# Performance work log

Measured on AMD Instinct MI355X. Metric: run time of the kernel, lower is better.

The kernel has to match this reference:

```python
import jax, jax.numpy as jnp
import numpy as np

B, S, D, K, R = 64, 512, 768, 8, 277
D_K = 64  # attention scale dim from original module (self.d_k)


def setup_inputs() -> dict:
    key = jax.random.key(0)
    ks = jax.random.split(key, 10)
    sc = 1.0 / np.sqrt(D)
    return {
        "embedding": jax.random.normal(ks[0], (B, S, D), dtype=jnp.float32),
        "h_span": jnp.sort(jax.random.randint(ks[1], (B, 2), 0, S), axis=-1).astype(jnp.int32),
        "t_span": jnp.sort(jax.random.randint(ks[2], (B, 2), 0, S), axis=-1).astype(jnp.int32),
        "b_spans": jnp.sort(jax.random.randint(ks[3], (B, K, 2), 0, S), axis=-1).astype(jnp.int32),
        "wu_w": jax.random.normal(ks[4], (D, D), dtype=jnp.float32) * sc,
        "wu_b": jnp.zeros((D,), jnp.float32),
        "wv_w": jax.random.normal(ks[5], (D, D), dtype=jnp.float32) * sc,
        "wv_b": jnp.zeros((D,), jnp.float32),
        "wi_w": jax.random.normal(ks[6], (D, D), dtype=jnp.float32) * sc,
        "wi_b": jnp.zeros((D,), jnp.float32),
        "ln1_w": jax.random.normal(ks[7], (D, D), dtype=jnp.float32) * sc,
        "ln1_b": jnp.zeros((D,), jnp.float32),
        "pred_w": jax.random.normal(ks[8], (R, D), dtype=jnp.float32) * sc,
        "pred_b": jnp.zeros((R,), jnp.float32),
    }


def _span_max(emb, span):
    # emb: [B, S, D]; span: [B, 2] inclusive [start, end] (start <= end).
    pos = jnp.arange(emb.shape[1])[None, :]          # [1, S]
    m = (pos >= span[:, :1]) & (pos <= span[:, 1:])  # [B, S]
    return jnp.max(jnp.where(m[:, :, None], emb, -jnp.inf), axis=1)  # [B, D]


def reference(embedding, h_span, t_span, b_spans,
              wu_w, wu_b, wv_w, wv_b, wi_w, wi_b,
              ln1_w, ln1_b, pred_w, pred_b):
    # Ragged entity-span max-pooling (torch.max over embedding[dp, s:e+1]).
    h_emb = _span_max(embedding, h_span)   # [B, D]
    t_emb = _span_max(embedding, t_span)   # [B, D]
    # K is a small fixed structural count (bridge subsampling cap); loop is fine.
    b_emb = jnp.stack([_span_max(embedding, b_spans[:, k, :]) for k in range(K)], axis=1)  # [B, K, D]

    # wu/wv/wi attention-style multi-hop path aggregation.
    u = h_emb @ wu_w.T + wu_b              # [B, D]
    v = t_emb @ wv_w.T + wv_b              # [B, D]
    bi = jnp.einsum('bkd,ed->bke', b_emb, wi_w) + wi_b  # [B, K, D]
    att = jax.nn.softmax(jnp.einsum('bd,bkd->bk', u, bi) / np.sqrt(D_K), axis=-1)  # [B, K]
    ctx = jnp.einsum('bk,bkd->bd', att, bi)  # [B, D]

    pair = jax.nn.relu((u + v + ctx) @ ln1_w.T + ln1_b)  # [B, D]
    logits = pair @ pred_w.T + pred_b                    # [B, R]
    return logits
```

## Files before the change

kernel.cpp:

```cpp
#include <hip/hip_runtime.h>
#include <hip/hip_bf16.h>

#define B 64
#define S 512
#define D 768
#define K 8
#define R 277
#define NSPAN 10
#define M_TOT 640

typedef unsigned short ushort_t;
typedef __attribute__((ext_vector_type(8))) short short8;
typedef __attribute__((ext_vector_type(4))) float f32x4;

__device__ __forceinline__ ushort_t f2bf(float f) {
    unsigned u = __float_as_uint(f);
    unsigned r = (u + 0x7FFFu + ((u >> 16) & 1u)) >> 16;
    return (ushort_t)r;
}

template<int RPC, int NCH>
__global__ void k_pool1(const float* __restrict__ emb,
                        const int* __restrict__ h_span,
                        const int* __restrict__ t_span,
                        const int* __restrict__ b_spans,
                        const float* __restrict__ wu,
                        const float* __restrict__ wv,
                        const float* __restrict__ wi,
                        float* __restrict__ partial,
                        ushort_t* __restrict__ wbf) {
    int b = blockIdx.x, c = blockIdx.y;
    int t = threadIdx.x;

    if (c >= NCH) {
        int g = (b * 18 + (c - NCH)) * 192 + t;
        const int per = (D*D) / 8;
        if (g < 3*per) {
            const float* src = (g < per) ? wu : (g < 2*per) ? wv : wi;
            int lg = g - ((g < per) ? 0 : (g < 2*per) ? per : 2*per);
            float4 f0 = *(const float4*)(src + (size_t)lg*8);
            float4 f1 = *(const float4*)(src + (size_t)lg*8 + 4);
            short8 o;
            o[0] = (short)f2bf(f0.x); o[1] = (short)f2bf(f0.y);
            o[2] = (short)f2bf(f0.z); o[3] = (short)f2bf(f0.w);
            o[4] = (short)f2bf(f1.x); o[5] = (short)f2bf(f1.y);
            o[6] = (short)f2bf(f1.z); o[7] = (short)f2bf(f1.w);
            *(short8*)&wbf[(size_t)g * 8] = o;
        }
        return;
    }

    int r0 = c * RPC;
    int s0[NSPAN], s1[NSPAN];
    s0[0] = h_span[b*2]; s1[0] = h_span[b*2+1];
    s0[1] = t_span[b*2]; s1[1] = t_span[b*2+1];
    #pragma unroll
    for (int k = 0; k < K; ++k) {
        s0[2+k] = b_spans[(b*K+k)*2];
        s1[2+k] = b_spans[(b*K+k)*2 + 1];
    }

    bool any = false;
    #pragma unroll
    for (int j = 0; j < NSPAN; ++j)
        any |= (s1[j] >= r0) && (s0[j] < r0 + RPC);
    if (!any) return;

    float4 m[NSPAN];
    #pragma unroll
    for (int j = 0; j < NSPAN; ++j)
        m[j] = make_float4(-INFINITY, -INFINITY, -INFINITY, -INFINITY);

    const float4* e4 = (const float4*)(emb + (size_t)b * S * D) + (size_t)r0 * (D/4) + t;
    #pragma unroll
    for (int i = 0; i < RPC; ++i) {
        float4 v = e4[i * (D/4)];
        int s = r0 + i;
        #pragma unroll
        for (int j = 0; j < NSPAN; ++j) {
            bool in = (s >= s0[j]) && (s <= s1[j]);
            float vx = in ? v.x : -INFINITY;
            float vy = in ? v.y : -INFINITY;
            float vz = in ? v.z : -INFINITY;
            float vw = in ? v.w : -INFINITY;
            m[j].x = fmaxf(m[j].x, vx); m[j].y = fmaxf(m[j].y, vy);
            m[j].z = fmaxf(m[j].z, vz); m[j].w = fmaxf(m[j].w, vw);
        }
    }

    #pragma unroll
    for (int j = 0; j < NSPAN; ++j) {
        if (s1[j] >= r0 && s0[j] < r0 + RPC) {
            *(float4*)(partial + (((size_t)(b*NCH + c))*NSPAN + j) * D + t*4) = m[j];
        }
    }
}

__global__ void k_pool2(const float* __restrict__ partial,
                        const int* __restrict__ h_span,
                        const int* __restrict__ t_span,
                        const int* __restrict__ b_spans,
                        ushort_t* __restrict__ pooled_bf, int rpc) {
    int task = blockIdx.x;
    int b = task / NSPAN, j = task % NSPAN;
    int s0, s1, row;
    if (j == 0)      { s0 = h_span[b*2]; s1 = h_span[b*2+1]; row = b; }
    else if (j == 1) { s0 = t_span[b*2]; s1 = t_span[b*2+1]; row = B + b; }
    else {
        int k = j - 2;
        s0 = b_spans[(b*K+k)*2]; s1 = b_spans[(b*K+k)*2 + 1];
        row = 2*B + b*K + k;
    }
    int nch = S / rpc;
    int c0 = s0 / rpc, c1 = s1 / rpc;
    int t = threadIdx.x;
    float4 m = make_float4(-INFINITY, -INFINITY, -INFINITY, -INFINITY);
    for (int c = c0; c <= c1; ++c) {
        float4 v = *(const float4*)(partial + (((size_t)(b*nch + c))*NSPAN + j) * D + t*4);
        m.x = fmaxf(m.x, v.x); m.y = fmaxf(m.y, v.y);
        m.z = fmaxf(m.z, v.z); m.w = fmaxf(m.w, v.w);
    }
    unsigned lo = (unsigned)f2bf(m.x) | ((unsigned)f2bf(m.y) << 16);
    unsigned hi = (unsigned)f2bf(m.z) | ((unsigned)f2bf(m.w) << 16);
    *(uint2*)&pooled_bf[(size_t)row * D + t*4] = make_uint2(lo, hi);
}

template<int KSPLIT>
__global__ __launch_bounds__(256)
void k_gemm_bf(const ushort_t* __restrict__ abf,
               const ushort_t* __restrict__ wbf,
               float* __restrict__ p_part) {
    __shared__ ushort_t Al[64][64];
    __shared__ ushort_t Bl[64][64];
    int e0 = blockIdx.x * 64;
    int m0 = blockIdx.y * 64;
    int dbase = blockIdx.z * (D / KSPLIT);
    const ushort_t* Wm = wbf + (size_t)((m0 < B) ? 0 : (m0 < 2*B) ? 1 : 2) * D * D;

    int tid = threadIdx.x;
    int w = tid >> 6, l = tid & 63;
    int srow = tid >> 2;
    int sc   = tid & 3;

    const ushort_t* ga = abf + (size_t)(m0 + srow) * D + dbase;
    const ushort_t* gb = Wm  + (size_t)(e0 + srow) * D + dbase;
    int p0 = ((sc     ) ^ (srow & 7)) * 8;
    int p1 = ((sc + 4 ) ^ (srow & 7)) * 8;

    f32x4 acc[4] = {};
    const int NIT = (D / KSPLIT) / 64;
    short8 pa0 = *(const short8*)(ga + sc*8);
    short8 pa1 = *(const short8*)(ga + sc*8 + 32);
    short8 pb0 = *(const short8*)(gb + sc*8);
    short8 pb1 = *(const short8*)(gb + sc*8 + 32);

    for (int it = 0; it < NIT; ++it) {
        __syncthreads();
        *(short8*)&Al[srow][p0] = pa0;
        *(short8*)&Al[srow][p1] = pa1;
        *(short8*)&Bl[srow][p0] = pb0;
        *(short8*)&Bl[srow][p1] = pb1;
        __syncthreads();
        if (it + 1 < NIT) {
            ga += 64; gb += 64;
            pa0 = *(const short8*)(ga + sc*8);
            pa1 = *(const short8*)(ga + sc*8 + 32);
            pb0 = *(const short8*)(gb + sc*8);
            pb1 = *(const short8*)(gb + sc*8 + 32);
        }
        int g = l >> 4, x = l & 7;
        #pragma unroll
        for (int ks = 0; ks < 2; ++ks) {
            int chunk = ks*4 + g;
            short8 a = *(const short8*)&Al[w*16 + (l & 15)][(chunk ^ x) * 8];
            #pragma unroll
            for (int nt = 0; nt < 4; ++nt) {
                short8 bf = *(const short8*)&Bl[nt*16 + (l & 15)][(chunk ^ x) * 8];
                acc[nt] = __builtin_amdgcn_mfma_f32_16x16x32_bf16(a, bf, acc[nt], 0, 0, 0);
            }
        }
    }

    int r4 = (l >> 4) * 4, cc = l & 15;
    #pragma unroll
    for (int nt = 0; nt < 4; ++nt)
        #pragma unroll
        for (int r = 0; r < 4; ++r)
            p_part[((size_t)blockIdx.z * M_TOT + m0 + w*16 + r4 + r) * D + e0 + nt*16 + cc] = acc[nt][r];
}

template<int KSPLIT>
__global__ __launch_bounds__(512)
void k_att2(const float* __restrict__ p_part,
            const float* __restrict__ wu_b,
            const float* __restrict__ wv_b,
            const float* __restrict__ wi_b,
            const float* __restrict__ pred_b,
            float* __restrict__ s_out,
            float* __restrict__ out) {
    __shared__ float U[D], V[D], BI[K][D];
    __shared__ float dots[K];
    int b = blockIdx.x, tid = threadIdx.x;

    for (int r = tid; r < R; r += 512) out[(size_t)b * R + r] = pred_b[r];

    for (int task = tid; task < NSPAN * (D/4); task += 512) {
        int j = task / (D/4), sl = task % (D/4);
        size_t row = (j == 0) ? (size_t)b : (j == 1) ? (size_t)(B + b)
                   : (size_t)(2*B + b*K + (j - 2));
        const float* bias = (j == 0) ? wu_b : (j == 1) ? wv_b : wi_b;
        float4 acc = *(const float4*)(bias + sl*4);
        #pragma unroll
        for (int ks = 0; ks < KSPLIT; ++ks) {
            float4 p = *(const float4*)(p_part + ((size_t)ks * M_TOT + row) * D + sl*4);
            acc.x += p.x; acc.y += p.y; acc.z += p.z; acc.w += p.w;
        }
        float* dst = (j == 0) ? U : (j == 1) ? V : BI[j-2];
        *(float4*)(dst + sl*4) = acc;
    }
    __syncthreads();

    int wave = tid >> 6, lane = tid & 63;
    {
        float part = 0.f;
        #pragma unroll
        for (int i = 0; i < D/64; ++i) {
            int d = i*64 + lane;
            part += U[d] * BI[wave][d];
        }
        #pragma unroll
        for (int off = 32; off > 0; off >>= 1) part += __shfl_xor(part, off);
        if (lane == 0) dots[wave] = part * 0.125f;
    }
    __syncthreads();

    float mx = -INFINITY;
    #pragma unroll
    for (int k = 0; k < K; ++k) mx = fmaxf(mx, dots[k]);
    float ex[K], sum = 0.f;
    #pragma unroll
    for (int k = 0; k < K; ++k) { ex[k] = expf(dots[k] - mx); sum += ex[k]; }
    float inv = 1.f / sum;
    for (int d = tid; d < D; d += 512) {
        float c = 0.f;
        #pragma unroll
        for (int k = 0; k < K; ++k) c += ex[k] * BI[k][d];
        s_out[(size_t)b * D + d] = U[d] + V[d] + c * inv;
    }
}

__device__ __forceinline__
void tile_fma(const float (*At)[68], const float (*Wt)[68],
              int tx, int ty, float acc[4][4]) {
    #pragma unroll
    for (int dd = 0; dd < 16; ++dd) {
        float4 av  = *(const float4*)&At[dd][ty << 2];
        float4 wvv = *(const float4*)&Wt[dd][tx << 2];
        float a_[4] = {av.x, av.y, av.z, av.w};
        float w_[4] = {wvv.x, wvv.y, wvv.z, wvv.w};
        #pragma unroll
        for (int i = 0; i < 4; ++i)
            #pragma unroll
            for (int jj = 0; jj < 4; ++jj)
                acc[i][jj] += a_[i] * w_[jj];
    }
}

template<int KS>
__global__ void k_pairg(const float* __restrict__ s,
                        const float* __restrict__ ln1_w,
                        float* __restrict__ pair_part) {
    __shared__ float At[16][68];
    __shared__ float Wt[16][68];
    int e0 = blockIdx.x * 64;
    int dbase = blockIdx.y * (D / KS);

    int tid = threadIdx.x;
    int tx = tid & 15, ty = tid >> 4;
    int lm = tid >> 2;
    int ld = (tid & 3) * 4;

    const float* arow = s     + (size_t)lm * D + ld + dbase;
    const float* wrow = ln1_w + (size_t)(e0 + lm) * D + ld + dbase;

    float acc[4][4] = {};
    const int NK = (D/KS) / 16;
    float4 a4 = *(const float4*)(arow);
    float4 w4 = *(const float4*)(wrow);
    for (int kc = 0; kc < NK; ++kc) {
        __syncthreads();
        At[ld+0][lm] = a4.x; At[ld+1][lm] = a4.y; At[ld+2][lm] = a4.z; At[ld+3][lm] = a4.w;
        Wt[ld+0][lm] = w4.x; Wt[ld+1][lm] = w4.y; Wt[ld+2][lm] = w4.z; Wt[ld+3][lm] = w4.w;
        __syncthreads();
        if (kc + 1 < NK) {
            a4 = *(const float4*)(arow + (kc+1)*16);
            w4 = *(const float4*)(wrow + (kc+1)*16);
        }
        tile_fma(At, Wt, tx, ty, acc);
    }
    #pragma unroll
    for (int i = 0; i < 4; ++i) {
        float4 o = make_float4(acc[i][0], acc[i][1], acc[i][2], acc[i][3]);
        *(float4*)(pair_part + ((size_t)blockIdx.y * B + ty*4 + i) * D + e0 + tx*4) = o;
    }
}

template<int KSP, int KSPAIR>
__global__ void k_predg(const float* __restrict__ pair_part,
                        const float* __restrict__ ln1_b,
                        const float* __restrict__ pred_w,
                        float* __restrict__ out) {
    __shared__ float At[16][68];
    __shared__ float Wt[16][68];
    int r0 = blockIdx.x * 64;
    int dbase = blockIdx.y * (D / KSP);

    int tid = threadIdx.x;
    int tx = tid & 15, ty = tid >> 4;
    int lm = tid >> 2;
    int ld = (tid & 3) * 4;

    int rw = r0 + lm; if (rw >= R) rw = R - 1;
    const float* prow = pair_part + (size_t)lm * D + ld + dbase;
    const float* wrow = pred_w + (size_t)rw * D + ld + dbase;

    auto build_a = [&](int kc) -> float4 {
        float4 a = *(const float4*)(ln1_b + dbase + kc*16 + ld);
        #pragma unroll
        for (int ks = 0; ks < KSPAIR; ++ks) {
            float4 p = *(const float4*)(prow + (size_t)ks * B * D + kc*16);
            a.x += p.x; a.y += p.y; a.z += p.z; a.w += p.w;
        }
        a.x = fmaxf(a.x, 0.f); a.y = fmaxf(a.y, 0.f);
        a.z = fmaxf(a.z, 0.f); a.w = fmaxf(a.w, 0.f);
        return a;
    };

    float acc[4][4] = {};
    const int NK = (D/KSP) / 16;
    float4 a4 = build_a(0);
    float4 w4 = *(const float4*)(wrow);
    for (int kc = 0; kc < NK; ++kc) {
        __syncthreads();
        At[ld+0][lm] = a4.x; At[ld+1][lm] = a4.y; At[ld+2][lm] = a4.z; At[ld+3][lm] = a4.w;
        Wt[ld+0][lm] = w4.x; Wt[ld+1][lm] = w4.y; Wt[ld+2][lm] = w4.z; Wt[ld+3][lm] = w4.w;
        __syncthreads();
        if (kc + 1 < NK) {
            a4 = build_a(kc+1);
            w4 = *(const float4*)(wrow + (kc+1)*16);
        }
        tile_fma(At, Wt, tx, ty, acc);
    }
    #pragma unroll
    for (int i = 0; i < 4; ++i) {
        int m = ty*4 + i;
        #pragma unroll
        for (int jj = 0; jj < 4; ++jj) {
            int r = r0 + tx*4 + jj;
            if (r < R) atomicAdd(&out[(size_t)m * R + r], acc[i][jj]);
        }
    }
}

extern "C" void kernel_launch(void* const* d_in, const int* in_sizes, int n_in,
                              void* d_out, int out_size, void* d_ws, size_t ws_size,
                              hipStream_t stream) {
    const float* emb     = (const float*)d_in[0];
    const int*   h_span  = (const int*)  d_in[1];
    const int*   t_span  = (const int*)  d_in[2];
    const int*   b_spans = (const int*)  d_in[3];
    const float* wu_w    = (const float*)d_in[4];
    const float* wu_b    = (const float*)d_in[5];
    const float* wv_w    = (const float*)d_in[6];
    const float* wv_b    = (const float*)d_in[7];
    const float* wi_w    = (const float*)d_in[8];
    const float* wi_b    = (const float*)d_in[9];
    const float* ln1_w   = (const float*)d_in[10];
    const float* ln1_b   = (const float*)d_in[11];
    const float* pred_w  = (const float*)d_in[12];
    const float* pred_b  = (const float*)d_in[13];
    float* out = (float*)d_out;

    const int KSPLIT = 2;
    const int KS     = 8;
    const int NCH    = 32;

    float* ws = (float*)d_ws;
    ushort_t* pooled_bf = (ushort_t*)ws;
    ushort_t* wbf   = (ushort_t*)(ws + (size_t)M_TOT*D/2);
    float* p_part    = ws + (size_t)M_TOT*D/2 + (size_t)3*D*D/2;
    float* s_buf     = p_part + (size_t)KSPLIT * M_TOT * D;
    float* pair_part = s_buf + (size_t)B * D;
    float* partial   = pair_part + (size_t)KS * B * D;
    (void)ws_size; (void)in_sizes; (void)n_in; (void)out_size;

    k_pool1<S/NCH, NCH><<<dim3(B, NCH + 18), 192, 0, stream>>>(
        emb, h_span, t_span, b_spans, wu_w, wv_w, wi_w, partial, wbf);
    k_pool2<<<M_TOT, 192, 0, stream>>>(partial, h_span, t_span, b_spans, pooled_bf, S / NCH);
    k_gemm_bf<KSPLIT><<<dim3(D/64, M_TOT/64, KSPLIT), 256, 0, stream>>>(pooled_bf, wbf, p_part);
    k_att2<KSPLIT><<<B, 512, 0, stream>>>(p_part, wu_b, wv_b, wi_b, pred_b, s_buf, out);
    k_pairg<KS><<<dim3(D/64, KS), 256, 0, stream>>>(s_buf, ln1_w, pair_part);
    k_predg<KS, KS><<<dim3((R+63)/64, KS), 256, 0, stream>>>(pair_part, ln1_b, pred_w, out);
}
```

Before: 66.07 us.

## Convert pair and prediction GEMMs to bf16 MFMA with fused weight conversion

Replaces the fp32 scalar-FMA tiled GEMMs for the ln1 and pred layers with bf16 MFMA kernels. The ln1_w and pred_w weights are converted to bf16 in the existing conversion blocks of the pooling kernel, and the attention output is now written as bf16. The split-K factors change to 6 and 12. The aim is to cut ALU time on the two tail GEMMs, at the cost of extra per-call conversion traffic and reduced precision.

After: 55.57 us. -15.9%, faster.

```diff
diff --git a/kernel.cpp b/kernel.cpp
--- a/kernel.cpp
+++ b/kernel.cpp
@@ -8,6 +8,7 @@
 #define R 277
 #define NSPAN 10
 #define M_TOT 640
+#define DD (D*D)
 
 typedef unsigned short ushort_t;
 typedef __attribute__((ext_vector_type(8))) short short8;
@@ -19,7 +20,7 @@
     return (ushort_t)r;
 }
 
-template<int RPC, int NCH>
+template<int RPC, int NCH, int CVTY>
 __global__ void k_pool1(const float* __restrict__ emb,
                         const int* __restrict__ h_span,
                         const int* __restrict__ t_span,
@@ -27,25 +28,32 @@
                         const float* __restrict__ wu,
                         const float* __restrict__ wv,
                         const float* __restrict__ wi,
+                        const float* __restrict__ ln1_w,
+                        const float* __restrict__ pred_w,
                         float* __restrict__ partial,
                         ushort_t* __restrict__ wbf) {
     int b = blockIdx.x, c = blockIdx.y;
     int t = threadIdx.x;
 
     if (c >= NCH) {
-        int g = (b * 18 + (c - NCH)) * 192 + t;
-        const int per = (D*D) / 8;
-        if (g < 3*per) {
-            const float* src = (g < per) ? wu : (g < 2*per) ? wv : wi;
-            int lg = g - ((g < per) ? 0 : (g < 2*per) ? per : 2*per);
-            float4 f0 = *(const float4*)(src + (size_t)lg*8);
-            float4 f1 = *(const float4*)(src + (size_t)lg*8 + 4);
+        int g = (b * CVTY + (c - NCH)) * 192 + t;
+        size_t e0 = (size_t)g * 8;
+        const size_t TOT = (size_t)4*DD + (size_t)R*D;
+        if (e0 < TOT) {
+            const float* src; size_t off;
+            if      (e0 < (size_t)DD)   { src = wu;     off = e0; }
+            else if (e0 < (size_t)2*DD) { src = wv;     off = e0 - DD; }
+            else if (e0 < (size_t)3*DD) { src = wi;     off = e0 - (size_t)2*DD; }
+            else if (e0 < (size_t)4*DD) { src = ln1_w;  off = e0 - (size_t)3*DD; }
+            else                        { src = pred_w; off = e0 - (size_t)4*DD; }
+            float4 f0 = *(const float4*)(src + off);
+            float4 f1 = *(const float4*)(src + off + 4);
             short8 o;
             o[0] = (short)f2bf(f0.x); o[1] = (short)f2bf(f0.y);
             o[2] = (short)f2bf(f0.z); o[3] = (short)f2bf(f0.w);
             o[4] = (short)f2bf(f1.x); o[5] = (short)f2bf(f1.y);
             o[6] = (short)f2bf(f1.z); o[7] = (short)f2bf(f1.w);
-            *(short8*)&wbf[(size_t)g * 8] = o;
+            *(short8*)&wbf[e0] = o;
         }
         return;
     }
@@ -135,7 +143,7 @@
     int e0 = blockIdx.x * 64;
     int m0 = blockIdx.y * 64;
     int dbase = blockIdx.z * (D / KSPLIT);
-    const ushort_t* Wm = wbf + (size_t)((m0 < B) ? 0 : (m0 < 2*B) ? 1 : 2) * D * D;
+    const ushort_t* Wm = wbf + (size_t)((m0 < B) ? 0 : (m0 < 2*B) ? 1 : 2) * DD;
 
     int tid = threadIdx.x;
     int w = tid >> 6, l = tid & 63;
@@ -196,7 +204,7 @@
             const float* __restrict__ wv_b,
             const float* __restrict__ wi_b,
             const float* __restrict__ pred_b,
-            float* __restrict__ s_out,
+            ushort_t* __restrict__ s_bf,
             float* __restrict__ out) {
     __shared__ float U[D], V[D], BI[K][D];
     __shared__ float dots[K];
@@ -245,119 +253,143 @@
         float c = 0.f;
         #pragma unroll
         for (int k = 0; k < K; ++k) c += ex[k] * BI[k][d];
-        s_out[(size_t)b * D + d] = U[d] + V[d] + c * inv;
-    }
-}
-
-__device__ __forceinline__
-void tile_fma(const float (*At)[68], const float (*Wt)[68],
-              int tx, int ty, float acc[4][4]) {
-    #pragma unroll
-    for (int dd = 0; dd < 16; ++dd) {
-        float4 av  = *(const float4*)&At[dd][ty << 2];
-        float4 wvv = *(const float4*)&Wt[dd][tx << 2];
-        float a_[4] = {av.x, av.y, av.z, av.w};
-        float w_[4] = {wvv.x, wvv.y, wvv.z, wvv.w};
-        #pragma unroll
-        for (int i = 0; i < 4; ++i)
+        s_bf[(size_t)b * D + d] = f2bf(U[d] + V[d] + c * inv);
+    }
+}
+
+template<int KSPL>
+__global__ __launch_bounds__(256)
+void k_pairg_bf(const ushort_t* __restrict__ s_bf,
+                const ushort_t* __restrict__ ln1_bf,
+                float* __restrict__ pair_part) {
+    __shared__ ushort_t Al[64][64];
+    __shared__ ushort_t Bl[64][64];
+    int e0 = blockIdx.x * 64;
+    int dbase = blockIdx.y * (D / KSPL);
+
+    int tid = threadIdx.x;
+    int w = tid >> 6, l = tid & 63;
+    int srow = tid >> 2;
+    int sc   = tid & 3;
+
+    const ushort_t* ga = s_bf   + (size_t)srow * D + dbase;
+    const ushort_t* gb = ln1_bf + (size_t)(e0 + srow) * D + dbase;
+    int p0 = ((sc     ) ^ (srow & 7)) * 8;
+    int p1 = ((sc + 4 ) ^ (srow & 7)) * 8;
+
+    f32x4 acc[4] = {};
+    const int NIT = (D / KSPL) / 64;
+    short8 pa0 = *(const short8*)(ga + sc*8);
+    short8 pa1 = *(const short8*)(ga + sc*8 + 32);
+    short8 pb0 = *(const short8*)(gb + sc*8);
+    short8 pb1 = *(const short8*)(gb + sc*8 + 32);
+
+    for (int it = 0; it < NIT; ++it) {
+        __syncthreads();
+        *(short8*)&Al[srow][p0] = pa0;
+        *(short8*)&Al[srow][p1] = pa1;
+        *(short8*)&Bl[srow][p0] = pb0;
+        *(short8*)&Bl[srow][p1] = pb1;
+        __syncthreads();
+        if (it + 1 < NIT) {
+            ga += 64; gb += 64;
+            pa0 = *(const short8*)(ga + sc*8);
+            pa1 = *(const short8*)(ga + sc*8 + 32);
+            pb0 = *(const short8*)(gb + sc*8);
+            pb1 = *(const short8*)(gb + sc*8 + 32);
+        }
+        int g = l >> 4, x = l & 7;
+        #pragma unroll
+        for (int ks = 0; ks < 2; ++ks) {
+            int chunk = ks*4 + g;
+            short8 a = *(const short8*)&Al[w*16 + (l & 15)][(chunk ^ x) * 8];
             #pragma unroll
-            for (int jj = 0; jj < 4; ++jj)
-                acc[i][jj] += a_[i] * w_[jj];
-    }
-}
-
-template<int KS>
-__global__ void k_pairg(const float* __restrict__ s,
-                        const float* __restrict__ ln1_w,
-                        float* __restrict__ pair_part) {
-    __shared__ float At[16][68];
-    __shared__ float Wt[16][68];
-    int e0 = blockIdx.x * 64;
-    int dbase = blockIdx.y * (D / KS);
+            for (int nt = 0; nt < 4; ++nt) {
+                short8 bf = *(const short8*)&Bl[nt*16 + (l & 15)][(chunk ^ x) * 8];
+                acc[nt] = __builtin_amdgcn_mfma_f32_16x16x32_bf16(a, bf, acc[nt], 0, 0, 0);
+            }
+        }
+    }
+
+    int r4 = (l >> 4) * 4, cc = l & 15;
+    #pragma unroll
+    for (int nt = 0; nt < 4; ++nt)
+        #pragma unroll
+        for (int r = 0; r < 4; ++r)
+            pair_part[((size_t)blockIdx.y * B + w*16 + r4 + r) * D + e0 + nt*16 + cc] = acc[nt][r];
+}
+
+template<int KSPP, int KSPL>
+__global__ __launch_bounds__(256)
+void k_predg_bf(const float* __restrict__ pair_part,
+                const float* __restrict__ ln1_b,
+                const ushort_t* __restrict__ pred_bf,
+                float* __restrict__ out) {
+    __shared__ ushort_t Al[64][64];
+    __shared__ ushort_t Bl[64][64];
+    int r0 = blockIdx.x * 64;
+    int dbase = blockIdx.y * (D / KSPP);
 
     int tid = threadIdx.x;
-    int tx = tid & 15, ty = tid >> 4;
-    int lm = tid >> 2;
-    int ld = (tid & 3) * 4;
-
-    const float* arow = s     + (size_t)lm * D + ld + dbase;
-    const float* wrow = ln1_w + (size_t)(e0 + lm) * D + ld + dbase;
-
-    float acc[4][4] = {};
-    const int NK = (D/KS) / 16;
-    float4 a4 = *(const float4*)(arow);
-    float4 w4 = *(const float4*)(wrow);
-    for (int kc = 0; kc < NK; ++kc) {
-        __syncthreads();
-        At[ld+0][lm] = a4.x; At[ld+1][lm] = a4.y; At[ld+2][lm] = a4.z; At[ld+3][lm] = a4.w;
-        Wt[ld+0][lm] = w4.x; Wt[ld+1][lm] = w4.y; Wt[ld+2][lm] = w4.z; Wt[ld+3][lm] = w4.w;
-        __syncthreads();
-        if (kc + 1 < NK) {
-            a4 = *(const float4*)(arow + (kc+1)*16);
-            w4 = *(const float4*)(wrow + (kc+1)*16);
-        }
-        tile_fma(At, Wt, tx, ty, acc);
-    }
-    #pragma unroll
-    for (int i = 0; i < 4; ++i) {
-        float4 o = make_float4(acc[i][0], acc[i][1], acc[i][2], acc[i][3]);
-        *(float4*)(pair_part + ((size_t)blockIdx.y * B + ty*4 + i) * D + e0 + tx*4) = o;
-    }
-}
-
-template<int KSP, int KSPAIR>
-__global__ void k_predg(const float* __restrict__ pair_part,
-                        const float* __restrict__ ln1_b,
-                        const float* __restrict__ pred_w,
-                        float* __restrict__ out) {
-    __shared__ float At[16][68];
-    __shared__ float Wt[16][68];
-    int r0 = blockIdx.x * 64;
-    int dbase = blockIdx.y * (D / KSP);
-
-    int tid = threadIdx.x;
-    int tx = tid & 15, ty = tid >> 4;
-    int lm = tid >> 2;
-    int ld = (tid & 3) * 4;
-
-    int rw = r0 + lm; if (rw >= R) rw = R - 1;
-    const float* prow = pair_part + (size_t)lm * D + ld + dbase;
-    const float* wrow = pred_w + (size_t)rw * D + ld + dbase;
-
-    auto build_a = [&](int kc) -> float4 {
-        float4 a = *(const float4*)(ln1_b + dbase + kc*16 + ld);
-        #pragma unroll
-        for (int ks = 0; ks < KSPAIR; ++ks) {
-            float4 p = *(const float4*)(prow + (size_t)ks * B * D + kc*16);
-            a.x += p.x; a.y += p.y; a.z += p.z; a.w += p.w;
-        }
-        a.x = fmaxf(a.x, 0.f); a.y = fmaxf(a.y, 0.f);
-        a.z = fmaxf(a.z, 0.f); a.w = fmaxf(a.w, 0.f);
-        return a;
+    int w = tid >> 6, l = tid & 63;
+    int srow = tid >> 2;
+    int sc   = tid & 3;
+    int p0 = ((sc     ) ^ (srow & 7)) * 8;
+    int p1 = ((sc + 4 ) ^ (srow & 7)) * 8;
+
+    auto build8 = [&](int off) -> short8 {
+        float4 a0 = *(const float4*)(ln1_b + dbase + off);
+        float4 a1 = *(const float4*)(ln1_b + dbase + off + 4);
+        #pragma unroll
+        for (int ks = 0; ks < KSPL; ++ks) {
+            const float* p = pair_part + ((size_t)ks * B + srow) * D + dbase + off;
+            float4 q0 = *(const float4*)p;
+            float4 q1 = *(const float4*)(p + 4);
+            a0.x += q0.x; a0.y += q0.y; a0.z += q0.z; a0.w += q0.w;
+            a1.x += q1.x; a1.y += q1.y; a1.z += q1.z; a1.w += q1.w;
+        }
+        short8 o;
+        o[0] = (short)f2bf(fmaxf(a0.x, 0.f)); o[1] = (short)f2bf(fmaxf(a0.y, 0.f));
+        o[2] = (short)f2bf(fmaxf(a0.z, 0.f)); o[3] = (short)f2bf(fmaxf(a0.w, 0.f));
+        o[4] = (short)f2bf(fmaxf(a1.x, 0.f)); o[5] = (short)f2bf(fmaxf(a1.y, 0.f));
+        o[6] = (short)f2bf(fmaxf(a1.z, 0.f)); o[7] = (short)f2bf(fmaxf(a1.w, 0.f));
+        return o;
     };
 
-    float acc[4][4] = {};
-    const int NK = (D/KSP) / 16;
-    float4 a4 = build_a(0);
-    float4 w4 = *(const float4*)(wrow);
-    for (int kc = 0; kc < NK; ++kc) {
-        __syncthreads();
-        At[ld+0][lm] = a4.x; At[ld+1][lm] = a4.y; At[ld+2][lm] = a4.z; At[ld+3][lm] = a4.w;
-        Wt[ld+0][lm] = w4.x; Wt[ld+1][lm] = w4.y; Wt[ld+2][lm] = w4.z; Wt[ld+3][lm] = w4.w;
-        __syncthreads();
-        if (kc + 1 < NK) {
-            a4 = build_a(kc+1);
-            w4 = *(const float4*)(wrow + (kc+1)*16);
-        }
-        tile_fma(At, Wt, tx, ty, acc);
-    }
-    #pragma unroll
-    for (int i = 0; i < 4; ++i) {
-        int m = ty*4 + i;
-        #pragma unroll
-        for (int jj = 0; jj < 4; ++jj) {
-            int r = r0 + tx*4 + jj;
-            if (r < R) atomicAdd(&out[(size_t)m * R + r], acc[i][jj]);
+    short8 a0 = build8(sc*8);
+    short8 a1 = build8(sc*8 + 32);
+    int rw = r0 + srow; if (rw >= R) rw = R - 1;
+    const ushort_t* gb = pred_bf + (size_t)rw * D + dbase;
+    short8 pb0 = *(const short8*)(gb + sc*8);
+    short8 pb1 = *(const short8*)(gb + sc*8 + 32);
+
+    *(short8*)&Al[srow][p0] = a0;
+    *(short8*)&Al[srow][p1] = a1;
+    *(short8*)&Bl[srow][p0] = pb0;
+    *(short8*)&Bl[srow][p1] = pb1;
+    __syncthreads();
+
+    f32x4 acc[4] = {};
+    int g = l >> 4, x = l & 7;
+    #pragma unroll
+    for (int ks = 0; ks < 2; ++ks) {
+        int chunk = ks*4 + g;
+        short8 a = *(const short8*)&Al[w*16 + (l & 15)][(chunk ^ x) * 8];
+        #pragma unroll
+        for (int nt = 0; nt < 4; ++nt) {
+            short8 bf = *(const short8*)&Bl[nt*16 + (l & 15)][(chunk ^ x) * 8];
+            acc[nt] = __builtin_amdgcn_mfma_f32_16x16x32_bf16(a, bf, acc[nt], 0, 0, 0);
+        }
+    }
+
+    int r4 = (l >> 4) * 4, cc = l & 15;
+    #pragma unroll
+    for (int nt = 0; nt < 4; ++nt) {
+        int rr = r0 + nt*16 + cc;
+        if (rr < R) {
+            #pragma unroll
+            for (int r = 0; r < 4; ++r)
+                atomicAdd(&out[(size_t)(w*16 + r4 + r) * R + rr], acc[nt][r]);
         }
     }
 }
@@ -382,23 +414,27 @@
     float* out = (float*)d_out;
 
     const int KSPLIT = 2;
-    const int KS     = 8;
+    const int KSPL   = 6;
+    const int KSPP   = 12;
     const int NCH    = 32;
+    const int CVTY   = 27;
 
     float* ws = (float*)d_ws;
     ushort_t* pooled_bf = (ushort_t*)ws;
-    ushort_t* wbf   = (ushort_t*)(ws + (size_t)M_TOT*D/2);
-    float* p_part    = ws + (size_t)M_TOT*D/2 + (size_t)3*D*D/2;
-    float* s_buf     = p_part + (size_t)KSPLIT * M_TOT * D;
-    float* pair_part = s_buf + (size_t)B * D;
-    float* partial   = pair_part + (size_t)KS * B * D;
+    ushort_t* wbf = (ushort_t*)(ws + (size_t)M_TOT*D/2);
+    size_t wbf_fl = ((size_t)4*DD + (size_t)R*D + 1) / 2;
+    float* p_part    = ws + (size_t)M_TOT*D/2 + wbf_fl;
+    ushort_t* s_bf   = (ushort_t*)(p_part + (size_t)KSPLIT*M_TOT*D);
+    float* pair_part = (float*)(s_bf + (size_t)B*D);
+    float* partial   = pair_part + (size_t)KSPL*B*D;
     (void)ws_size; (void)in_sizes; (void)n_in; (void)out_size;
 
-    k_pool1<S/NCH, NCH><<<dim3(B, NCH + 18), 192, 0, stream>>>(
-        emb, h_span, t_span, b_spans, wu_w, wv_w, wi_w, partial, wbf);
+    k_pool1<S/NCH, NCH, CVTY><<<dim3(B, NCH + CVTY), 192, 0, stream>>>(
+        emb, h_span, t_span, b_spans, wu_w, wv_w, wi_w, ln1_w, pred_w, partial, wbf);
     k_pool2<<<M_TOT, 192, 0, stream>>>(partial, h_span, t_span, b_spans, pooled_bf, S / NCH);
     k_gemm_bf<KSPLIT><<<dim3(D/64, M_TOT/64, KSPLIT), 256, 0, stream>>>(pooled_bf, wbf, p_part);
-    k_att2<KSPLIT><<<B, 512, 0, stream>>>(p_part, wu_b, wv_b, wi_b, pred_b, s_buf, out);
-    k_pairg<KS><<<dim3(D/64, KS), 256, 0, stream>>>(s_buf, ln1_w, pair_part);
-    k_predg<KS, KS><<<dim3((R+63)/64, KS), 256, 0, stream>>>(pair_part, ln1_b, pred_w, out);
-}
+    k_att2<KSPLIT><<<B, 512, 0, stream>>>(p_part, wu_b, wv_b, wi_b, pred_b, s_bf, out);
+    k_pairg_bf<KSPL><<<dim3(D/64, KSPL), 256, 0, stream>>>(s_bf, wbf + (size_t)3*DD, pair_part);
+    k_predg_bf<KSPP, KSPL><<<dim3((R+63)/64, KSPP), 256, 0, stream>>>(
+        pair_part, ln1_b, wbf + (size_t)4*DD, out);
+}
```
